# Performance work log

Measured on AMD Instinct MI355X. Metric: run time of the kernel, lower is better.

The kernel has to match this reference:

```python
import jax, jax.numpy as jnp
import numpy as np

G = 16          # horizontal stripes
K = 4           # latents per stripe
TEMP = 0.125
TOPK_RATIO = 0.125
GATE_THR = 0.05
EPS = 1e-6
KSZ = 3


def setup_inputs() -> dict:
    key = jax.random.key(0)
    k1, k2 = jax.random.split(key)
    x = jax.random.normal(k1, (64, 256, 64, 44), dtype=jnp.float32)
    latent_basis = jax.random.normal(k2, (G, K, 256), dtype=jnp.float32)
    return {"x": x, "latent_basis": latent_basis}


def _avg_pool3(x):
    # x: [n, g, c, sh, w]; 3x3 avg pool, stride 1, pad 1, count_include_pad=True
    s = jax.lax.reduce_window(x, 0.0, jax.lax.add,
                              (1, 1, 1, KSZ, KSZ), (1, 1, 1, 1, 1),
                              [(0, 0), (0, 0), (0, 0), (1, 1), (1, 1)])
    return s / float(KSZ * KSZ)


def _l2norm(v, axis=-1):
    return v / jnp.maximum(jnp.linalg.norm(v, axis=axis, keepdims=True), 1e-12)


def reference(x, latent_basis):
    n, c, h, w = x.shape
    sh = h // G
    p = sh * w
    # split into horizontal stripes: [n, g, c, sh, w]
    xr = x.reshape(n, c, G, sh, w).transpose(0, 2, 1, 3, 4)
    support_feat = _avg_pool3(xr)
    feat_flat = xr.transpose(0, 1, 3, 4, 2).reshape(n, G, p, c)          # ngpc
    support_flat = support_feat.transpose(0, 1, 3, 4, 2).reshape(n, G, p, c)

    # active mask from detached feature energy
    e = jax.lax.stop_gradient(xr).astype(jnp.float32)
    fe = jnp.mean(e * e, axis=2)                                          # n g sh w
    fe = fe / jnp.maximum(jnp.max(fe, axis=(-2, -1), keepdims=True), EPS)
    active = (fe > GATE_THR).astype(jnp.float32)
    fallback = (fe > 0).astype(jnp.float32)
    use_fb = jnp.sum(active, axis=(-2, -1), keepdims=True) <= 0
    active = jnp.where(use_fb, fallback, active).reshape(n, G, p)

    # cosine-similarity routing
    sfn = _l2norm(support_flat)
    lbn = _l2norm(latent_basis)                                           # g k c
    logits = jnp.einsum('ngpc,gkc->ngpk', sfn, lbn) / TEMP
    route_prob = jax.nn.softmax(logits, axis=-1)
    support = route_prob * active[..., None]                              # n g p k
    pool_w = support / jnp.maximum(jnp.sum(support, axis=2, keepdims=True), EPS)
    tokens = jnp.einsum('ngpk,ngpc->ngkc', pool_w, feat_flat)
    tokens = tokens.transpose(0, 3, 1, 2).reshape(n, c, G * K)            # n c (g k)

    # top-k presence
    kk = max(1, min(p, int(p * TOPK_RATIO)))
    topv, _ = jax.lax.top_k(support.transpose(0, 1, 3, 2), kk)            # n g k kk
    presence = jnp.mean(topv, axis=-1).reshape(n, G * K)
    presence = presence / jnp.maximum(jnp.sum(presence, axis=1, keepdims=True), EPS)

    # scatter per-stripe maps back into full-resolution zero tensors
    eye = jnp.eye(G, dtype=support.dtype)
    loc_s = support.reshape(n, G, sh, w, K).transpose(0, 1, 4, 2, 3)      # n g k sh w
    loc_p = pool_w.reshape(n, G, sh, w, K).transpose(0, 1, 4, 2, 3)
    smap = jnp.einsum('ngksw,gG->ngkGsw', loc_s, eye).reshape(n, G * K, h, w)
    pmap = jnp.einsum('ngksw,gG->ngkGsw', loc_p, eye).reshape(n, G * K, h, w)
    support_flat_global = smap.transpose(0, 2, 3, 1).reshape(n, h * w, G * K)
    pool_weights_flat_global = pmap.transpose(0, 2, 3, 1).reshape(n, h * w, G * K)

    return (tokens.astype(x.dtype), presence.astype(x.dtype),
            support_flat_global.astype(x.dtype), pool_weights_flat_global.astype(x.dtype))
```

## Files before the change

### kernel.cpp

```cpp
#include <hip/hip_runtime.h>
#include <math.h>

#define GG   16
#define KK   4
#define NN   64
#define CC   256
#define SHH  4
#define WW   44
#define PP   176
#define HWSZ 2816
#define CHW  720896
#define TOPKK 22

template<int CTRL, int RMASK>
__device__ __forceinline__ float dpp0(float v) {
    return __int_as_float(__builtin_amdgcn_update_dpp(
        0, __float_as_int(v), CTRL, RMASK, 0xF, true));
}
__device__ __forceinline__ float nbrL(float v) { return dpp0<0x138, 0xF>(v); }
__device__ __forceinline__ float nbrR(float v) { return dpp0<0x130, 0xF>(v); }

__device__ __forceinline__ float wave_sum63(float v) {
    v += dpp0<0x111, 0xF>(v);
    v += dpp0<0x112, 0xF>(v);
    v += dpp0<0x114, 0xF>(v);
    v += dpp0<0x118, 0xF>(v);
    v += dpp0<0x142, 0xA>(v);
    v += dpp0<0x143, 0xC>(v);
    return v;
}
__device__ __forceinline__ float bcast63(float v) {
    return __int_as_float(__builtin_amdgcn_readlane(__float_as_int(v), 63));
}
__device__ __forceinline__ float wave_sum_all(float v) { return bcast63(wave_sum63(v)); }

__device__ __forceinline__ float wave_max_nn(float v) {
    v = fmaxf(v, dpp0<0x111, 0xF>(v));
    v = fmaxf(v, dpp0<0x112, 0xF>(v));
    v = fmaxf(v, dpp0<0x114, 0xF>(v));
    v = fmaxf(v, dpp0<0x118, 0xF>(v));
    v = fmaxf(v, dpp0<0x142, 0xA>(v));
    v = fmaxf(v, dpp0<0x143, 0xC>(v));
    return bcast63(v);
}

__global__ __launch_bounds__(64) void norm_basis_kernel(
    const float* __restrict__ lb, float* __restrict__ lbn) {
    const int gk = blockIdx.x;
    const int lane = threadIdx.x;
    const float* row = lb + (size_t)gk * CC;
    float v0 = row[lane], v1 = row[lane + 64], v2 = row[lane + 128], v3 = row[lane + 192];
    float ss = v0 * v0 + v1 * v1 + v2 * v2 + v3 * v3;
    float tot = wave_sum_all(ss);
    float sc = (1.0f / 9.0f) / fmaxf(sqrtf(tot), 1e-12f);
    const int g = gk >> 2, k = gk & 3;
    float* dst = lbn + (size_t)g * CC * 4 + k;
    dst[(size_t)lane * 4]         = v0 * sc;
    dst[(size_t)(lane + 64) * 4]  = v1 * sc;
    dst[(size_t)(lane + 128) * 4] = v2 * sc;
    dst[(size_t)(lane + 192) * 4] = v3 * sc;
}

__global__ __launch_bounds__(512, 8) void routing_kernel(
    const float* __restrict__ x, const float* __restrict__ lbn,
    float* __restrict__ sup_ws, float* __restrict__ pw_ws,
    float* __restrict__ pres_ws) {
    const int g = blockIdx.x;
    const int n = blockIdx.y;
    const int tid = threadIdx.x;
    const int w = __builtin_amdgcn_readfirstlane(tid >> 6);
    const int lane = tid & 63;
    const bool al = lane < WW;

    __shared__ float4 pd[8][PP];
    __shared__ float2 pnf[8][PP];
    __shared__ float redA[4], redB[4], zred[4][4];
    float4* sup4 = pd[2];
    float4* pw4  = pd[4];

    const float* xb = x + (size_t)n * CHW + g * PP;
    const int c0 = w * 32;
    const float4* lbq = (const float4*)lbn + (g << 8) + c0;

    float4 dk[4];
    float nr[4] = {0, 0, 0, 0}, fe[4] = {0, 0, 0, 0};
    #pragma unroll
    for (int s = 0; s < 4; ++s) dk[s] = make_float4(0, 0, 0, 0);

    const float* xp = xb + (size_t)c0 * HWSZ + lane;
    float r0 = 0, r1 = 0, r2 = 0, r3 = 0;
    if (al) { r0 = xp[0]; r1 = xp[44]; r2 = xp[88]; r3 = xp[132]; }
    xp += HWSZ;
    #pragma unroll 1
    for (int i = 0; i < 32; ++i) {
        float b0 = 0, b1 = 0, b2 = 0, b3 = 0;
        if (i < 31 && al) { b0 = xp[0]; b1 = xp[44]; b2 = xp[88]; b3 = xp[132]; }
        xp += HWSZ;
        float4 lbv = lbq[i];
        fe[0] += r0 * r0; fe[1] += r1 * r1; fe[2] += r2 * r2; fe[3] += r3 * r3;
        float h0 = r0 + nbrL(r0) + nbrR(r0);
        float h1 = r1 + nbrL(r1) + nbrR(r1);
        float h2 = r2 + nbrL(r2) + nbrR(r2);
        float h3 = r3 + nbrL(r3) + nbrR(r3);
        float p0 = h0 + h1;
        float p1 = p0 + h2;
        float t23 = h2 + h3;
        float p2 = h1 + t23;
        float p3 = t23;
        nr[0] += p0 * p0; nr[1] += p1 * p1; nr[2] += p2 * p2; nr[3] += p3 * p3;
        dk[0].x += p0 * lbv.x; dk[0].y += p0 * lbv.y; dk[0].z += p0 * lbv.z; dk[0].w += p0 * lbv.w;
        dk[1].x += p1 * lbv.x; dk[1].y += p1 * lbv.y; dk[1].z += p1 * lbv.z; dk[1].w += p1 * lbv.w;
        dk[2].x += p2 * lbv.x; dk[2].y += p2 * lbv.y; dk[2].z += p2 * lbv.z; dk[2].w += p2 * lbv.w;
        dk[3].x += p3 * lbv.x; dk[3].y += p3 * lbv.y; dk[3].z += p3 * lbv.z; dk[3].w += p3 * lbv.w;
        r0 = b0; r1 = b1; r2 = b2; r3 = b3;
    }
    if (al) {
        #pragma unroll
        for (int s = 0; s < 4; ++s) {
            pd[w][s * 44 + lane]  = dk[s];
            pnf[w][s * 44 + lane] = make_float2(nr[s], fe[s]);
        }
    }
    __syncthreads();

    if (tid < PP) {
        float4 a = pd[0][tid];
        #pragma unroll
        for (int ww = 1; ww < 8; ++ww) {
            float4 b = pd[ww][tid];
            a.x += b.x; a.y += b.y; a.z += b.z; a.w += b.w;
        }
        pd[0][tid] = a;
    } else if (tid >= 256 && tid < 256 + PP) {
        const int p = tid - 256;
        float2 a = pnf[0][p];
        #pragma unroll
        for (int ww = 1; ww < 8; ++ww) {
            float2 b = pnf[ww][p];
            a.x += b.x; a.y += b.y;
        }
        pnf[0][p] = a;
    }
    __syncthreads();

    const int s4 = w & 3;
    const int pix = s4 * 44 + (al ? lane : 0);
    float4 dv = pd[0][pix];
    float2 nf = pnf[0][pix];
    float nrm = nf.x;
    float fev = nf.y * (1.0f / 256.0f);

    float fmw = wave_max_nn(al ? fev : 0.0f);
    if (w < 4 && lane == 0) redA[s4] = fmw;
    __syncthreads();
    float femax = fmaxf(fmaxf(redA[0], redA[1]), fmaxf(redA[2], redA[3]));
    float den = fmaxf(femax, 1e-6f);
    bool pa = al && ((fev / den) > 0.05f);
    unsigned long long bl = __ballot((int)pa);
    if (w < 4 && lane == 0) redB[s4] = (float)__popcll(bl);
    __syncthreads();
    float cnt = redB[0] + redB[1] + redB[2] + redB[3];
    float actv = pa ? 1.0f : 0.0f;
    if (cnt <= 0.0f) actv = (al && (fev > 0.0f)) ? 1.0f : 0.0f;

    float inv = 72.0f / fmaxf(sqrtf(nrm), 9e-12f);
    float L0 = dv.x * inv, L1 = dv.y * inv, L2 = dv.z * inv, L3 = dv.w * inv;
    float mx = fmaxf(fmaxf(L0, L1), fmaxf(L2, L3));
    float e0 = expf(L0 - mx), e1 = expf(L1 - mx), e2 = expf(L2 - mx), e3 = expf(L3 - mx);
    float esum = e0 + e1 + e2 + e3;
    float sc = actv / esum;
    float s0 = e0 * sc, s1 = e1 * sc, s2 = e2 * sc, s3 = e3 * sc;

    float z0 = wave_sum63(s0), z1 = wave_sum63(s1), z2 = wave_sum63(s2), z3 = wave_sum63(s3);
    if (w < 4 && lane == 63) { zred[s4][0] = z0; zred[s4][1] = z1; zred[s4][2] = z2; zred[s4][3] = z3; }
    __syncthreads();
    float Z0 = zred[0][0] + zred[1][0] + zred[2][0] + zred[3][0];
    float Z1 = zred[0][1] + zred[1][1] + zred[2][1] + zred[3][1];
    float Z2 = zred[0][2] + zred[1][2] + zred[2][2] + zred[3][2];
    float Z3 = zred[0][3] + zred[1][3] + zred[2][3] + zred[3][3];
    float q0 = s0 / fmaxf(Z0, 1e-6f);
    float q1 = s1 / fmaxf(Z1, 1e-6f);
    float q2 = s2 / fmaxf(Z2, 1e-6f);
    float q3 = s3 / fmaxf(Z3, 1e-6f);

    if (w < 4 && al) {
        float4 sv = make_float4(s0, s1, s2, s3);
        float4 qv = make_float4(q0, q1, q2, q3);
        sup4[pix] = sv;
        pw4[pix]  = qv;
        const size_t wsb = (size_t)(n * GG + g) * PP + pix;
        ((float4*)sup_ws)[wsb] = sv;
        ((float4*)pw_ws)[wsb]  = qv;
    }
    __syncthreads();

    if (w < 4) {
        const float* supf = (const float*)sup4;
        const int k = w;
        float v0 = supf[lane * 4 + k];
        float v1 = supf[(lane + 64) * 4 + k];
        float v2 = (lane < PP - 128) ? supf[(lane + 128) * 4 + k] : -1e30f;
        float tks = 0.0f;
        for (int it = 0; it < TOPKK; ++it) {
            float lm = fmaxf(v0, fmaxf(v1, v2));
            float M = wave_max_nn(lm);
            tks += M;
            unsigned long long mk = __ballot((int)(lm == M));
            int src = __ffsll(mk) - 1;
            if (lane == src) {
                if (v0 == M)      v0 = -1e30f;
                else if (v1 == M) v1 = -1e30f;
                else              v2 = -1e30f;
            }
        }
        if (lane == 0) pres_ws[(size_t)n * 64 + g * KK + k] = tks * (1.0f / (float)TOPKK);
    }
}

__global__ __launch_bounds__(256, 8) void token_kernel(
    const float* __restrict__ x, const float* __restrict__ pw_ws,
    float* __restrict__ tok_out) {
    const int g = blockIdx.x & 15;
    const int chunk = blockIdx.x >> 4;
    const int n = blockIdx.y;
    const int w = __builtin_amdgcn_readfirstlane(threadIdx.x >> 6);
    const int lane = threadIdx.x & 63;

    const float4* pwq = (const float4*)pw_ws + (size_t)(n * GG + g) * PP;
    float4 pwa = pwq[lane];
    float4 pwb = pwq[lane + 64];
    float4 pwc = (lane < 48) ? pwq[lane + 128] : make_float4(0, 0, 0, 0);

    const int cb = chunk * 64 + w * 16;
    const float* xp = x + (size_t)n * CHW + g * PP + (size_t)cb * HWSZ + lane;
    float* tokg = tok_out + (size_t)n * CC * 64 + g * KK + (size_t)cb * 64;

    float a0 = xp[0];
    float a1 = xp[64];
    float a2 = (lane < 48) ? xp[128] : 0.0f;
    xp += HWSZ;
    #pragma unroll 1
    for (int i = 0; i < 16; ++i) {
        float b0 = 0, b1 = 0, b2 = 0;
        if (i < 15) {
            b0 = xp[0]; b1 = xp[64];
            if (lane < 48) b2 = xp[128];
        }
        xp += HWSZ;
        float t0 = a0 * pwa.x + a1 * pwb.x + a2 * pwc.x;
        float t1 = a0 * pwa.y + a1 * pwb.y + a2 * pwc.y;
        float t2 = a0 * pwa.z + a1 * pwb.z + a2 * pwc.z;
        float t3 = a0 * pwa.w + a1 * pwb.w + a2 * pwc.w;
        t0 = wave_sum63(t0); t1 = wave_sum63(t1); t2 = wave_sum63(t2); t3 = wave_sum63(t3);
        if (lane == 63) {
            *(float4*)(tokg + (size_t)i * 64) = make_float4(t0, t1, t2, t3);
        }
        a0 = b0; a1 = b1; a2 = b2;
    }
}

__global__ __launch_bounds__(256, 8) void scatter_kernel(
    const float4* __restrict__ sup_ws4, const float4* __restrict__ pw_ws4,
    float4* __restrict__ outS, float4* __restrict__ outP) {
    const int g = blockIdx.x;
    const int n = blockIdx.y;
    const int t = threadIdx.x;
    __shared__ float4 ls[PP], lp[PP];
    const size_t wsb = (size_t)(n * GG + g) * PP;
    if (t < PP) { ls[t] = sup_ws4[wsb + t]; lp[t] = pw_ws4[wsb + t]; }
    __syncthreads();
    const size_t obase = ((size_t)n * HWSZ + (size_t)g * PP) * 16;
    const float4 z = make_float4(0, 0, 0, 0);
    #pragma unroll 1
    for (int j = t; j < PP * 16; j += 256) {
        const int px = j >> 4, q = j & 15;
        const bool hit = (q == g);
        outS[obase + j] = hit ? ls[px] : z;
        outP[obase + j] = hit ? lp[px] : z;
    }
}

__global__ __launch_bounds__(64) void presence_kernel(
    const float* __restrict__ pres_ws, float* __restrict__ outp) {
    const int n = blockIdx.x;
    const int lane = threadIdx.x;
    float v = pres_ws[(size_t)n * 64 + lane];
    float tot = wave_sum_all(v);
    outp[(size_t)n * 64 + lane] = v / fmaxf(tot, 1e-6f);
}

extern "C" void kernel_launch(void* const* d_in, const int* in_sizes, int n_in,
                              void* d_out, int out_size, void* d_ws, size_t ws_size,
                              hipStream_t stream) {
    const float* x = (const float*)d_in[0];
    const float* lb = (const float*)d_in[1];
    float* ws = (float*)d_ws;
    float* lbn     = ws;
    float* pres_ws = lbn + 16384;
    float* sup_ws  = pres_ws + 4096;
    float* pw_ws   = sup_ws + 720896;

    float* out = (float*)d_out;
    float* tok  = out;
    float* pres = out + 1048576;
    float* outS = out + 1052672;
    float* outP = outS + 11534336;

    norm_basis_kernel<<<GG * KK, 64, 0, stream>>>(lb, lbn);
    routing_kernel<<<dim3(GG, NN), 512, 0, stream>>>(x, lbn, sup_ws, pw_ws, pres_ws);
    token_kernel<<<dim3(GG * 4, NN), 256, 0, stream>>>(x, pw_ws, tok);
    scatter_kernel<<<dim3(GG, NN), 256, 0, stream>>>(
        (const float4*)sup_ws, (const float4*)pw_ws, (float4*)outS, (float4*)outP);
    presence_kernel<<<NN, 64, 0, stream>>>(pres_ws, pres);
}
```

Measured before the change: 342.6 us.

## Fuse basis normalization into routing and merge token and scatter kernels

Basis normalization moves into the routing kernel: each block normalizes its stripe's four latent rows into shared memory, so the separate launch and the global round trip go away. The token and scatter kernels are merged into one 512-thread kernel that reuses the shared-memory pool weights, with each wave now covering 32 channels. The routing loop also prefetches two channels ahead to hide load latency. In exchange, every routing block repeats the small normalization work, and the token stage now runs with fewer blocks, each doing more work.

```diff
diff --git a/kernel.cpp b/kernel.cpp
--- a/kernel.cpp
+++ b/kernel.cpp
@@ -44,25 +44,8 @@
     return bcast63(v);
 }
 
-__global__ __launch_bounds__(64) void norm_basis_kernel(
-    const float* __restrict__ lb, float* __restrict__ lbn) {
-    const int gk = blockIdx.x;
-    const int lane = threadIdx.x;
-    const float* row = lb + (size_t)gk * CC;
-    float v0 = row[lane], v1 = row[lane + 64], v2 = row[lane + 128], v3 = row[lane + 192];
-    float ss = v0 * v0 + v1 * v1 + v2 * v2 + v3 * v3;
-    float tot = wave_sum_all(ss);
-    float sc = (1.0f / 9.0f) / fmaxf(sqrtf(tot), 1e-12f);
-    const int g = gk >> 2, k = gk & 3;
-    float* dst = lbn + (size_t)g * CC * 4 + k;
-    dst[(size_t)lane * 4]         = v0 * sc;
-    dst[(size_t)(lane + 64) * 4]  = v1 * sc;
-    dst[(size_t)(lane + 128) * 4] = v2 * sc;
-    dst[(size_t)(lane + 192) * 4] = v3 * sc;
-}
-
 __global__ __launch_bounds__(512, 8) void routing_kernel(
-    const float* __restrict__ x, const float* __restrict__ lbn,
+    const float* __restrict__ x, const float* __restrict__ lb_raw,
     float* __restrict__ sup_ws, float* __restrict__ pw_ws,
     float* __restrict__ pres_ws) {
     const int g = blockIdx.x;
@@ -74,13 +57,27 @@
 
     __shared__ float4 pd[8][PP];
     __shared__ float2 pnf[8][PP];
+    __shared__ float4 lbn_lds[CC];
     __shared__ float redA[4], redB[4], zred[4][4];
     float4* sup4 = pd[2];
     float4* pw4  = pd[4];
 
+    if (w < 4) {
+        const float* row = lb_raw + ((size_t)g * KK + w) * CC;
+        float v0 = row[lane], v1 = row[lane + 64], v2 = row[lane + 128], v3 = row[lane + 192];
+        float ss = v0 * v0 + v1 * v1 + v2 * v2 + v3 * v3;
+        float tot = wave_sum_all(ss);
+        float sc = (1.0f / 9.0f) / fmaxf(sqrtf(tot), 1e-12f);
+        float* dst = (float*)lbn_lds;
+        dst[lane * 4 + w]         = v0 * sc;
+        dst[(lane + 64) * 4 + w]  = v1 * sc;
+        dst[(lane + 128) * 4 + w] = v2 * sc;
+        dst[(lane + 192) * 4 + w] = v3 * sc;
+    }
+    __syncthreads();
+
     const float* xb = x + (size_t)n * CHW + g * PP;
     const int c0 = w * 32;
-    const float4* lbq = (const float4*)lbn + (g << 8) + c0;
 
     float4 dk[4];
     float nr[4] = {0, 0, 0, 0}, fe[4] = {0, 0, 0, 0};
@@ -88,20 +85,24 @@
     for (int s = 0; s < 4; ++s) dk[s] = make_float4(0, 0, 0, 0);
 
     const float* xp = xb + (size_t)c0 * HWSZ + lane;
-    float r0 = 0, r1 = 0, r2 = 0, r3 = 0;
-    if (al) { r0 = xp[0]; r1 = xp[44]; r2 = xp[88]; r3 = xp[132]; }
-    xp += HWSZ;
+    float c0r = 0, c1r = 0, c2r = 0, c3r = 0;
+    float n0r = 0, n1r = 0, n2r = 0, n3r = 0;
+    if (al) {
+        c0r = xp[0]; c1r = xp[44]; c2r = xp[88]; c3r = xp[132];
+        n0r = xp[HWSZ]; n1r = xp[HWSZ + 44]; n2r = xp[HWSZ + 88]; n3r = xp[HWSZ + 132];
+    }
+    xp += 2 * HWSZ;
     #pragma unroll 1
     for (int i = 0; i < 32; ++i) {
-        float b0 = 0, b1 = 0, b2 = 0, b3 = 0;
-        if (i < 31 && al) { b0 = xp[0]; b1 = xp[44]; b2 = xp[88]; b3 = xp[132]; }
+        float f0 = 0, f1 = 0, f2 = 0, f3 = 0;
+        if (i < 30 && al) { f0 = xp[0]; f1 = xp[44]; f2 = xp[88]; f3 = xp[132]; }
         xp += HWSZ;
-        float4 lbv = lbq[i];
-        fe[0] += r0 * r0; fe[1] += r1 * r1; fe[2] += r2 * r2; fe[3] += r3 * r3;
-        float h0 = r0 + nbrL(r0) + nbrR(r0);
-        float h1 = r1 + nbrL(r1) + nbrR(r1);
-        float h2 = r2 + nbrL(r2) + nbrR(r2);
-        float h3 = r3 + nbrL(r3) + nbrR(r3);
+        float4 lbv = lbn_lds[c0 + i];
+        fe[0] += c0r * c0r; fe[1] += c1r * c1r; fe[2] += c2r * c2r; fe[3] += c3r * c3r;
+        float h0 = c0r + nbrL(c0r) + nbrR(c0r);
+        float h1 = c1r + nbrL(c1r) + nbrR(c1r);
+        float h2 = c2r + nbrL(c2r) + nbrR(c2r);
+        float h3 = c3r + nbrL(c3r) + nbrR(c3r);
         float p0 = h0 + h1;
         float p1 = p0 + h2;
         float t23 = h2 + h3;
@@ -112,7 +113,8 @@
         dk[1].x += p1 * lbv.x; dk[1].y += p1 * lbv.y; dk[1].z += p1 * lbv.z; dk[1].w += p1 * lbv.w;
         dk[2].x += p2 * lbv.x; dk[2].y += p2 * lbv.y; dk[2].z += p2 * lbv.z; dk[2].w += p2 * lbv.w;
         dk[3].x += p3 * lbv.x; dk[3].y += p3 * lbv.y; dk[3].z += p3 * lbv.z; dk[3].w += p3 * lbv.w;
-        r0 = b0; r1 = b1; r2 = b2; r3 = b3;
+        c0r = n0r; c1r = n1r; c2r = n2r; c3r = n3r;
+        n0r = f0; n1r = f1; n2r = f2; n3r = f3;
     }
     if (al) {
         #pragma unroll
@@ -217,66 +219,64 @@
     }
 }
 
-__global__ __launch_bounds__(256, 8) void token_kernel(
-    const float* __restrict__ x, const float* __restrict__ pw_ws,
-    float* __restrict__ tok_out) {
-    const int g = blockIdx.x & 15;
-    const int chunk = blockIdx.x >> 4;
-    const int n = blockIdx.y;
-    const int w = __builtin_amdgcn_readfirstlane(threadIdx.x >> 6);
-    const int lane = threadIdx.x & 63;
-
-    const float4* pwq = (const float4*)pw_ws + (size_t)(n * GG + g) * PP;
-    float4 pwa = pwq[lane];
-    float4 pwb = pwq[lane + 64];
-    float4 pwc = (lane < 48) ? pwq[lane + 128] : make_float4(0, 0, 0, 0);
-
-    const int cb = chunk * 64 + w * 16;
-    const float* xp = x + (size_t)n * CHW + g * PP + (size_t)cb * HWSZ + lane;
-    float* tokg = tok_out + (size_t)n * CC * 64 + g * KK + (size_t)cb * 64;
-
-    float a0 = xp[0];
-    float a1 = xp[64];
-    float a2 = (lane < 48) ? xp[128] : 0.0f;
-    xp += HWSZ;
-    #pragma unroll 1
-    for (int i = 0; i < 16; ++i) {
-        float b0 = 0, b1 = 0, b2 = 0;
-        if (i < 15) {
-            b0 = xp[0]; b1 = xp[64];
-            if (lane < 48) b2 = xp[128];
-        }
-        xp += HWSZ;
-        float t0 = a0 * pwa.x + a1 * pwb.x + a2 * pwc.x;
-        float t1 = a0 * pwa.y + a1 * pwb.y + a2 * pwc.y;
-        float t2 = a0 * pwa.z + a1 * pwb.z + a2 * pwc.z;
-        float t3 = a0 * pwa.w + a1 * pwb.w + a2 * pwc.w;
-        t0 = wave_sum63(t0); t1 = wave_sum63(t1); t2 = wave_sum63(t2); t3 = wave_sum63(t3);
-        if (lane == 63) {
-            *(float4*)(tokg + (size_t)i * 64) = make_float4(t0, t1, t2, t3);
-        }
-        a0 = b0; a1 = b1; a2 = b2;
-    }
-}
-
-__global__ __launch_bounds__(256, 8) void scatter_kernel(
+__global__ __launch_bounds__(512, 8) void tokscat_kernel(
+    const float* __restrict__ x,
     const float4* __restrict__ sup_ws4, const float4* __restrict__ pw_ws4,
-    float4* __restrict__ outS, float4* __restrict__ outP) {
+    float* __restrict__ tok_out, float4* __restrict__ outS, float4* __restrict__ outP) {
     const int g = blockIdx.x;
     const int n = blockIdx.y;
-    const int t = threadIdx.x;
+    const int tid = threadIdx.x;
+    const int w = __builtin_amdgcn_readfirstlane(tid >> 6);
+    const int lane = tid & 63;
+
     __shared__ float4 ls[PP], lp[PP];
     const size_t wsb = (size_t)(n * GG + g) * PP;
-    if (t < PP) { ls[t] = sup_ws4[wsb + t]; lp[t] = pw_ws4[wsb + t]; }
-    __syncthreads();
-    const size_t obase = ((size_t)n * HWSZ + (size_t)g * PP) * 16;
-    const float4 z = make_float4(0, 0, 0, 0);
-    #pragma unroll 1
-    for (int j = t; j < PP * 16; j += 256) {
-        const int px = j >> 4, q = j & 15;
-        const bool hit = (q == g);
-        outS[obase + j] = hit ? ls[px] : z;
-        outP[obase + j] = hit ? lp[px] : z;
+    if (tid < PP) ls[tid] = sup_ws4[wsb + tid];
+    else if (tid >= 256 && tid < 256 + PP) lp[tid - 256] = pw_ws4[wsb + tid - 256];
+    __syncthreads();
+
+    {
+        const size_t obase = ((size_t)n * HWSZ + (size_t)g * PP) * 16;
+        const float4 z = make_float4(0, 0, 0, 0);
+        #pragma unroll 1
+        for (int j = tid; j < PP * 16; j += 512) {
+            const int px = j >> 4, q = j & 15;
+            const bool hit = (q == g);
+            outS[obase + j] = hit ? ls[px] : z;
+            outP[obase + j] = hit ? lp[px] : z;
+        }
+    }
+
+    {
+        float4 pwa = lp[lane];
+        float4 pwb = lp[lane + 64];
+        float4 pwc = (lane < 48) ? lp[lane + 128] : make_float4(0, 0, 0, 0);
+        const int cb = w * 32;
+        const float* xp = x + (size_t)n * CHW + g * PP + (size_t)cb * HWSZ + lane;
+        float* tokg = tok_out + (size_t)n * CC * 64 + g * KK + (size_t)cb * 64;
+
+        float a0 = xp[0];
+        float a1 = xp[64];
+        float a2 = (lane < 48) ? xp[128] : 0.0f;
+        xp += HWSZ;
+        #pragma unroll 1
+        for (int i = 0; i < 32; ++i) {
+            float b0 = 0, b1 = 0, b2 = 0;
+            if (i < 31) {
+                b0 = xp[0]; b1 = xp[64];
+                if (lane < 48) b2 = xp[128];
+            }
+            xp += HWSZ;
+            float t0 = a0 * pwa.x + a1 * pwb.x + a2 * pwc.x;
+            float t1 = a0 * pwa.y + a1 * pwb.y + a2 * pwc.y;
+            float t2 = a0 * pwa.z + a1 * pwb.z + a2 * pwc.z;
+            float t3 = a0 * pwa.w + a1 * pwb.w + a2 * pwc.w;
+            t0 = wave_sum63(t0); t1 = wave_sum63(t1); t2 = wave_sum63(t2); t3 = wave_sum63(t3);
+            if (lane == 63) {
+                *(float4*)(tokg + (size_t)i * 64) = make_float4(t0, t1, t2, t3);
+            }
+            a0 = b0; a1 = b1; a2 = b2;
+        }
     }
 }
 
@@ -295,8 +295,7 @@
     const float* x = (const float*)d_in[0];
     const float* lb = (const float*)d_in[1];
     float* ws = (float*)d_ws;
-    float* lbn     = ws;
-    float* pres_ws = lbn + 16384;
+    float* pres_ws = ws;
     float* sup_ws  = pres_ws + 4096;
     float* pw_ws   = sup_ws + 720896;
 
@@ -306,10 +305,8 @@
     float* outS = out + 1052672;
     float* outP = outS + 11534336;
 
-    norm_basis_kernel<<<GG * KK, 64, 0, stream>>>(lb, lbn);
-    routing_kernel<<<dim3(GG, NN), 512, 0, stream>>>(x, lbn, sup_ws, pw_ws, pres_ws);
-    token_kernel<<<dim3(GG * 4, NN), 256, 0, stream>>>(x, pw_ws, tok);
-    scatter_kernel<<<dim3(GG, NN), 256, 0, stream>>>(
-        (const float4*)sup_ws, (const float4*)pw_ws, (float4*)outS, (float4*)outP);
+    routing_kernel<<<dim3(GG, NN), 512, 0, stream>>>(x, lb, sup_ws, pw_ws, pres_ws);
+    tokscat_kernel<<<dim3(GG, NN), 512, 0, stream>>>(
+        x, (const float4*)sup_ws, (const float4*)pw_ws, tok, (float4*)outS, (float4*)outP);
     presence_kernel<<<NN, 64, 0, stream>>>(pres_ws, pres);
 }
```

Result: slower. 351.7 us (+2.7%).
